# Kernel tuning notes

Measured on AMD Instinct MI355X. Metric: run time of the kernel, lower is better.

## Reference

```python
import jax, jax.numpy as jnp
import numpy as np

B, H, W, C = 8, 64, 64, 512
DQK = C // 8  # query/key channel dim from Conv2D(filters//8, 1)


def setup_inputs() -> dict:
    key = jax.random.key(0)
    ks = jax.random.split(key, 8)
    s_in = 1.0 / np.sqrt(C)
    x = jax.random.normal(ks[0], (B, H, W, C), dtype=jnp.float32)
    Wq = jax.random.normal(ks[1], (C, DQK), dtype=jnp.float32) * s_in
    bq = jnp.zeros((DQK,), dtype=jnp.float32)
    Wk = jax.random.normal(ks[2], (C, DQK), dtype=jnp.float32) * s_in
    bk = jnp.zeros((DQK,), dtype=jnp.float32)
    Wv = jax.random.normal(ks[3], (C, C), dtype=jnp.float32) * s_in
    bv = jnp.zeros((C,), dtype=jnp.float32)
    # gamma initialized to zeros in the original, but use a nonzero value so
    # the attention branch actually contributes to the output/gradients.
    gamma = jnp.ones((1,), dtype=jnp.float32) * 0.5
    return {"x": x, "Wq": Wq, "bq": bq, "Wk": Wk, "bk": bk,
            "Wv": Wv, "bv": bv, "gamma": gamma}


def reference(x, Wq, bq, Wk, bk, Wv, bv, gamma):
    b, h, w, c = x.shape
    n = h * w  # spatial_size
    xf = x.reshape(b, n, c)
    # 1x1 convs == per-pixel channel matmuls
    q = xf @ Wq + bq            # [B, N, C//8]
    k = xf @ Wk + bk            # [B, N, C//8]
    v = xf @ Wv + bv            # [B, N, C]
    # Dot(axes=-1): attn[b,i,j] = sum_d q[b,i,d] * k[b,j,d]
    attn = jnp.einsum('bid,bjd->bij', q, k)
    attn = jax.nn.softmax(attn, axis=-1)
    # Dot(axes=-2): out[b,j,c] = sum_i attn[b,i,j] * v[b,i,c]  (note transpose)
    out = jnp.einsum('bij,bic->bjc', attn, v)
    out = out.reshape(b, h, w, c)
    return gamma * out + x
```

## Files before the change

### kernel.cpp

```cpp
#include <hip/hip_runtime.h>
#include <hip/hip_bf16.h>
#include <cstdio>

typedef unsigned short u16;
typedef __attribute__((ext_vector_type(4))) float f32x4;
typedef __attribute__((ext_vector_type(8))) short s16x8;

#define LOG2E 1.4426950408889634f

__device__ __forceinline__ u16 bf16b(float f) {
  union { float f; unsigned u; } c; c.f = f;
  unsigned u = c.u;
  return (u16)((u + 0x7FFFu + ((u >> 16) & 1u)) >> 16);
}

__device__ __forceinline__ void load16(const void* g, void* l) {
  __builtin_amdgcn_global_load_lds(
      (const __attribute__((address_space(1))) void*)g,
      (__attribute__((address_space(3))) void*)l, 16, 0, 0);
}


__global__ __launch_bounds__(256) void cvt_all_k(const float* __restrict__ x,
                                                 const float* __restrict__ Wq,
                                                 const float* __restrict__ Wk,
                                                 const float* __restrict__ Wv,
                                                 u16* __restrict__ xb,
                                                 u16* __restrict__ Wcat) {
  int bid = blockIdx.x;
  if (bid < 16384) {
    long i = ((long)bid * 256 + threadIdx.x) * 4;
    float4 f = *(const float4*)&x[i];
    unsigned lo = (unsigned)bf16b(f.x) | ((unsigned)bf16b(f.y) << 16);
    unsigned hi = (unsigned)bf16b(f.z) | ((unsigned)bf16b(f.w) << 16);
    uint2 v; v.x = lo; v.y = hi;
    *(uint2*)&xb[i] = v;
  } else {
    int idx = (bid - 16384) * 256 + threadIdx.x;
    int nn = idx >> 9, k = idx & 511;
    float v;
    if (nn < 64)       v = Wq[k * 64 + nn];
    else if (nn < 128) v = Wk[k * 64 + (nn - 64)];
    else               v = Wv[k * 512 + (nn - 128)];
    Wcat[idx] = bf16b(v);
  }
}

__global__ __launch_bounds__(256, 2) void projGemm(
    const u16* __restrict__ A, const u16* __restrict__ B,
    u16* __restrict__ Qb, u16* __restrict__ Kb, u16* __restrict__ Vt,
    const float* __restrict__ bq, const float* __restrict__ bk,
    const float* __restrict__ bv) {
  constexpr int BM = 128, BN = 128, FM = 4, FN = 4;
  __shared__ __align__(16) u16 At[BM * 64];
  __shared__ __align__(16) u16 Bt[BN * 64];
  const int tid = threadIdx.x;
  const int lane = tid & 63, w = tid >> 6;
  const int wr = w >> 1, wc = w & 1;
  const int l15 = lane & 15, lhi = lane >> 4;
  const long m0 = (long)blockIdx.x * BM;
  const long n0 = (long)blockIdx.y * BN;

  f32x4 acc[FM][FN] = {};

  for (int k0 = 0; k0 < 512; k0 += 64) {
#pragma unroll
    for (int it = 0; it < 8; ++it) {
      int q = it * 256 + tid;
      if (q < BM * 8) {
        int row = q >> 3, c8 = q & 7;
        load16(A + (m0 + row) * 512 + k0 + c8 * 8, &At[q * 8]);
      } else {
        int q2 = q - BM * 8;
        int row = q2 >> 3, c8 = q2 & 7;
        load16(B + (n0 + row) * 512 + k0 + c8 * 8, &Bt[q2 * 8]);
      }
    }
    __syncthreads();
#pragma unroll
    for (int kk = 0; kk < 64; kk += 32) {
      s16x8 af[FM], bf[FN];
#pragma unroll
      for (int i = 0; i < FM; ++i)
        af[i] = *(const s16x8*)&At[(wr * 64 + i * 16 + l15) * 64 + kk + lhi * 8];
#pragma unroll
      for (int j = 0; j < FN; ++j)
        bf[j] = *(const s16x8*)&Bt[(wc * 64 + j * 16 + l15) * 64 + kk + lhi * 8];
#pragma unroll
      for (int i = 0; i < FM; ++i)
#pragma unroll
        for (int j = 0; j < FN; ++j)
          acc[i][j] = __builtin_amdgcn_mfma_f32_16x16x32_bf16(af[i], bf[j],
                                                              acc[i][j], 0, 0, 0);
    }
    __syncthreads();
  }

#pragma unroll
  for (int i = 0; i < FM; ++i) {
#pragma unroll
    for (int j = 0; j < FN; ++j) {
      long mm = m0 + wr * 64 + i * 16 + lhi * 4;
      long nn = n0 + wc * 64 + j * 16 + l15;
      if (nn < 64) {
        float bb = bq[nn];
#pragma unroll
        for (int r = 0; r < 4; ++r)
          Qb[(mm + r) * 64 + nn] = bf16b(acc[i][j][r] + bb);
      } else if (nn < 128) {
        float bb = bk[nn - 64];
#pragma unroll
        for (int r = 0; r < 4; ++r)
          Kb[(mm + r) * 64 + nn - 64] = bf16b(acc[i][j][r] + bb);
      } else {
        long c = nn - 128;
        float bb = bv[c];
        unsigned u01 = (unsigned)bf16b(acc[i][j][0] + bb) |
                       ((unsigned)bf16b(acc[i][j][1] + bb) << 16);
        unsigned u23 = (unsigned)bf16b(acc[i][j][2] + bb) |
                       ((unsigned)bf16b(acc[i][j][3] + bb) << 16);
        uint2 u; u.x = u01; u.y = u23;
        *(uint2*)&Vt[(mm >> 12) * 512 * 4096 + c * 4096 + (mm & 4095)] = u;
      }
    }
  }
}

__global__ __launch_bounds__(256, 2) void stats_k(const u16* __restrict__ Qb,
                                                  const u16* __restrict__ Kb,
                                                  float* __restrict__ m_part,
                                                  float* __restrict__ l_part) {
  const int b = blockIdx.z, jc = blockIdx.y;
  const long i0 = (long)blockIdx.x * 128;
  const u16* Q = Qb + (long)b * 4096 * 64;
  const u16* Kp = Kb + (long)b * 4096 * 64;
  __shared__ __align__(16) u16 Qt[128 * 64];
  __shared__ __align__(16) u16 Kt[128 * 64];
  const int tid = threadIdx.x, lane = tid & 63, w = tid >> 6;
  const int l15 = lane & 15, lhi = lane >> 4;

#pragma unroll
  for (int it = 0; it < 4; ++it) {
    int q = it * 256 + tid;
    int row = q >> 3, c8 = q & 7;
    load16(Q + (i0 + row) * 64 + c8 * 8, &Qt[q * 8]);
  }

  float mrun[2][4], lrun[2][4];
#pragma unroll
  for (int i = 0; i < 2; ++i)
#pragma unroll
    for (int r = 0; r < 4; ++r) { mrun[i][r] = -1e30f; lrun[i][r] = 0.f; }

  for (int jt = 0; jt < 8; ++jt) {
    long j0 = (long)jc * 1024 + jt * 128;
#pragma unroll
    for (int it = 0; it < 4; ++it) {
      int q = it * 256 + tid;
      int row = q >> 3, c8 = q & 7;
      load16(Kp + (j0 + row) * 64 + c8 * 8, &Kt[q * 8]);
    }
    __syncthreads();
    f32x4 acc[2][8] = {};
#pragma unroll
    for (int kk = 0; kk < 64; kk += 32) {
      s16x8 af[2], bf[8];
#pragma unroll
      for (int i = 0; i < 2; ++i)
        af[i] = *(const s16x8*)&Qt[(w * 32 + i * 16 + l15) * 64 + kk + lhi * 8];
#pragma unroll
      for (int j = 0; j < 8; ++j)
        bf[j] = *(const s16x8*)&Kt[(j * 16 + l15) * 64 + kk + lhi * 8];
#pragma unroll
      for (int i = 0; i < 2; ++i)
#pragma unroll
        for (int j = 0; j < 8; ++j)
          acc[i][j] = __builtin_amdgcn_mfma_f32_16x16x32_bf16(af[i], bf[j],
                                                              acc[i][j], 0, 0, 0);
    }
#pragma unroll
    for (int i = 0; i < 2; ++i)
#pragma unroll
      for (int r = 0; r < 4; ++r) {
        float tm = acc[i][0][r];
#pragma unroll
        for (int j = 1; j < 8; ++j) tm = fmaxf(tm, acc[i][j][r]);
        float mo = mrun[i][r];
        float mn = fmaxf(mo, tm);
        float s = 0.f;
#pragma unroll
        for (int j = 0; j < 8; ++j) s += __expf(acc[i][j][r] - mn);
        lrun[i][r] = lrun[i][r] * __expf(mo - mn) + s;
        mrun[i][r] = mn;
      }
    __syncthreads();
  }

#pragma unroll
  for (int i = 0; i < 2; ++i)
#pragma unroll
    for (int r = 0; r < 4; ++r) {
      float m = mrun[i][r], l = lrun[i][r];
#pragma unroll
      for (int d = 1; d < 16; d <<= 1) {
        float mo = __shfl_xor(m, d);
        float lo = __shfl_xor(l, d);
        float mn = fmaxf(m, mo);
        l = l * __expf(m - mn) + lo * __expf(mo - mn);
        m = mn;
      }
      if (l15 == 0) {
        long ig = i0 + w * 32 + i * 16 + lhi * 4 + r;
        long idx = ((long)(b * 4 + jc)) * 4096 + ig;
        m_part[idx] = m;
        l_part[idx] = l;
      }
    }
}

__global__ __launch_bounds__(256) void merge_k(const float* __restrict__ m_part,
                                               const float* __restrict__ l_part,
                                               float* __restrict__ mfin) {
  int idx = blockIdx.x * 256 + threadIdx.x;
  int b = idx >> 12, i = idx & 4095;
  float m = -1e30f, l = 0.f;
#pragma unroll
  for (int jc = 0; jc < 4; ++jc) {
    long o = ((long)(b * 4 + jc)) * 4096 + i;
    float mp = m_part[o], lp = l_part[o];
    float mn = fmaxf(m, mp);
    l = l * __expf(m - mn) + lp * __expf(mp - mn);
    m = mn;
  }
  mfin[idx] = fmaf(m, LOG2E, __log2f(l));
}

__global__ __launch_bounds__(512, 2) void fusedPV(
    const u16* __restrict__ Qb, const u16* __restrict__ Kb,
    const u16* __restrict__ Vt, const float* __restrict__ mfin,
    const float* __restrict__ x, const float* __restrict__ gamma,
    float* __restrict__ out) {
  __shared__ __align__(16) u16 Vc[2][512 * 64];
  __shared__ __align__(16) u16 Pl[2][128 * 64];
  const int tid = threadIdx.x, lane = tid & 63, w = tid >> 6;
  const int l15 = lane & 15, lhi = lane >> 4;
  const int wi = w & 1, wj = w >> 1;
  const int wjj = w & 1, wcc = w >> 1;
  const int s = blockIdx.x + 32 * blockIdx.z;
  const int pi = (s & 7) * 32 + (s >> 3);
  const int b = pi >> 5;
  const long j0 = (long)(pi & 31) * 128;
  const u16* Qg = Qb + (long)b * 4096 * 64;
  const u16* Kg = Kb + (long)b * 4096 * 64;
  const u16* Vg = Vt + (long)b * 512 * 4096;
  const float* mg = mfin + (long)b * 4096;
  const float gma = gamma[0];

#pragma unroll
  for (int p = 0; p < 2; ++p) {
    int q = p * 512 + tid;
    int r = q >> 3, col = q & 7, cg = col ^ (r & 7);
    load16(Kg + (j0 + r) * 64 + cg * 8,
           (char*)&Pl[0][0] + r * 128 + col * 16);
  }
  asm volatile("s_waitcnt vmcnt(0) lgkmcnt(0)\n\ts_barrier" ::: "memory");
  s16x8 kf[2][2];
#pragma unroll
  for (int fj = 0; fj < 2; ++fj)
#pragma unroll
    for (int kx = 0; kx < 2; ++kx) {
      int r = wj * 32 + fj * 16 + l15;
      kf[fj][kx] = *(const s16x8*)((const char*)&Pl[0][0] + r * 128 +
                                   (((kx * 32 + lhi * 8) * 2) ^ ((r & 7) << 4)));
    }
  __syncthreads();

  f32x4 acc2[4][8] = {};
  s16x8 qf[2][2];
  f32x4 mv[2];

#pragma unroll
  for (int fi = 0; fi < 2; ++fi) {
#pragma unroll
    for (int kx = 0; kx < 2; ++kx)
      qf[fi][kx] = *(const s16x8*)&Qg[(long)(wi * 32 + fi * 16 + l15) * 64 +
                                      kx * 32 + lhi * 8];
    mv[fi] = *(const f32x4*)&mg[wi * 32 + fi * 16 + lhi * 4];
  }
#pragma unroll
  for (int p = 0; p < 8; ++p) {
    int q = p * 512 + tid;
    int r = q >> 3, col = q & 7, cg = col ^ (r & 7);
    load16(Vg + (long)r * 4096 + cg * 8,
           (char*)&Vc[0][0] + r * 128 + col * 16);
  }
#pragma unroll
  for (int fi = 0; fi < 2; ++fi) {
    f32x4 a1[2] = {};
#pragma unroll
    for (int kx = 0; kx < 2; ++kx)
#pragma unroll
      for (int fj = 0; fj < 2; ++fj)
        a1[fj] = __builtin_amdgcn_mfma_f32_16x16x32_bf16(qf[fi][kx],
                                                         kf[fj][kx], a1[fj],
                                                         0, 0, 0);
    const int i0l = wi * 32 + fi * 16 + lhi * 4;
#pragma unroll
    for (int fj = 0; fj < 2; ++fj) {
      int j = wj * 32 + fj * 16 + l15;
      float p0 = __builtin_amdgcn_exp2f(fmaf(a1[fj][0], LOG2E, -mv[fi][0]));
      float p1 = __builtin_amdgcn_exp2f(fmaf(a1[fj][1], LOG2E, -mv[fi][1]));
      float p2 = __builtin_amdgcn_exp2f(fmaf(a1[fj][2], LOG2E, -mv[fi][2]));
      float p3 = __builtin_amdgcn_exp2f(fmaf(a1[fj][3], LOG2E, -mv[fi][3]));
      uint2 u;
      u.x = (unsigned)bf16b(p0) | ((unsigned)bf16b(p1) << 16);
      u.y = (unsigned)bf16b(p2) | ((unsigned)bf16b(p3) << 16);
      *(uint2*)((char*)&Pl[0][0] + j * 128 + ((i0l * 2) ^ ((j & 7) << 4))) = u;
    }
  }

  for (int t = 0; t < 64; ++t) {
    const char* plc = (const char*)&Pl[t & 1][0];
    char* pln = (char*)&Pl[(t + 1) & 1][0];
    const char* vcc = (const char*)&Vc[t & 1][0];
    asm volatile("s_waitcnt vmcnt(0) lgkmcnt(0)\n\ts_barrier" ::: "memory");
    if (t < 63) {
      const long i2 = (long)(t + 1) * 64;
#pragma unroll
      for (int fi = 0; fi < 2; ++fi) {
#pragma unroll
        for (int kx = 0; kx < 2; ++kx)
          qf[fi][kx] = *(const s16x8*)&Qg[(i2 + wi * 32 + fi * 16 + l15) * 64 +
                                          kx * 32 + lhi * 8];
        mv[fi] = *(const f32x4*)&mg[i2 + wi * 32 + fi * 16 + lhi * 4];
      }
#pragma unroll
      for (int p = 0; p < 8; ++p) {
        int q = p * 512 + tid;
        int r = q >> 3, col = q & 7, cg = col ^ (r & 7);
        load16(Vg + (long)r * 4096 + i2 + cg * 8,
               (char*)&Vc[(t + 1) & 1][0] + r * 128 + col * 16);
      }
    }
    __builtin_amdgcn_sched_barrier(0);
    __builtin_amdgcn_s_setprio(1);
#pragma unroll
    for (int kx = 0; kx < 2; ++kx) {
      s16x8 pa[4];
#pragma unroll
      for (int fm = 0; fm < 4; ++fm) {
        int r = wjj * 64 + fm * 16 + l15;
        pa[fm] = *(const s16x8*)(plc + r * 128 +
                                 (((kx * 32 + lhi * 8) * 2) ^ ((r & 7) << 4)));
      }
#pragma unroll
      for (int fn = 0; fn < 8; ++fn) {
        int r = wcc * 128 + fn * 16 + l15;
        s16x8 vb = *(const s16x8*)(vcc + r * 128 +
                                   (((kx * 32 + lhi * 8) * 2) ^ ((r & 7) << 4)));
#pragma unroll
        for (int fm = 0; fm < 4; ++fm)
          acc2[fm][fn] = __builtin_amdgcn_mfma_f32_16x16x32_bf16(
              pa[fm], vb, acc2[fm][fn], 0, 0, 0);
      }
    }
    __builtin_amdgcn_s_setprio(0);
    if (t < 63) {
#pragma unroll
      for (int fi = 0; fi < 2; ++fi) {
        f32x4 a1[2] = {};
#pragma unroll
        for (int kx = 0; kx < 2; ++kx)
#pragma unroll
          for (int fj = 0; fj < 2; ++fj)
            a1[fj] = __builtin_amdgcn_mfma_f32_16x16x32_bf16(qf[fi][kx],
                                                             kf[fj][kx],
                                                             a1[fj], 0, 0, 0);
        const int i0l = wi * 32 + fi * 16 + lhi * 4;
#pragma unroll
        for (int fj = 0; fj < 2; ++fj) {
          int j = wj * 32 + fj * 16 + l15;
          float p0 = __builtin_amdgcn_exp2f(fmaf(a1[fj][0], LOG2E, -mv[fi][0]));
          float p1 = __builtin_amdgcn_exp2f(fmaf(a1[fj][1], LOG2E, -mv[fi][1]));
          float p2 = __builtin_amdgcn_exp2f(fmaf(a1[fj][2], LOG2E, -mv[fi][2]));
          float p3 = __builtin_amdgcn_exp2f(fmaf(a1[fj][3], LOG2E, -mv[fi][3]));
          uint2 u;
          u.x = (unsigned)bf16b(p0) | ((unsigned)bf16b(p1) << 16);
          u.y = (unsigned)bf16b(p2) | ((unsigned)bf16b(p3) << 16);
          *(uint2*)(pln + j * 128 + ((i0l * 2) ^ ((j & 7) << 4))) = u;
        }
      }
    }
  }

#pragma unroll
  for (int fm = 0; fm < 4; ++fm) {
#pragma unroll
    for (int fn = 0; fn < 8; ++fn) {
      long j = j0 + wjj * 64 + fm * 16 + lhi * 4;
      long c = wcc * 128 + fn * 16 + l15;
#pragma unroll
      for (int r = 0; r < 4; ++r) {
        long o = ((long)b * 4096 + j + r) * 512 + c;
        out[o] = gma * acc2[fm][fn][r] + x[o];
      }
    }
  }
}


extern "C" void kernel_launch(void* const* d_in, const int* in_sizes, int n_in,
                              void* d_out, int out_size, void* d_ws,
                              size_t ws_size, hipStream_t stream) {
  const float* x = (const float*)d_in[0];
  const float* Wq = (const float*)d_in[1];
  const float* bq = (const float*)d_in[2];
  const float* Wk = (const float*)d_in[3];
  const float* bk = (const float*)d_in[4];
  const float* Wv = (const float*)d_in[5];
  const float* bv = (const float*)d_in[6];
  const float* gamma = (const float*)d_in[7];
  float* out = (float*)d_out;

  char* ws = (char*)d_ws;
  size_t off = 0;
  auto alloc = [&](size_t bytes) {
    char* p = ws + off;
    off += (bytes + 255) & ~(size_t)255;
    return p;
  };
  u16* xb = (u16*)alloc((size_t)32768 * 512 * 2);
  u16* Wcat = (u16*)alloc((size_t)640 * 512 * 2);
  u16* Qb = (u16*)alloc((size_t)8 * 4096 * 64 * 2);
  u16* Kb = (u16*)alloc((size_t)8 * 4096 * 64 * 2);
  u16* Vt = (u16*)alloc((size_t)8 * 512 * 4096 * 2);
  float* m_part = (float*)alloc((size_t)8 * 4 * 4096 * 4);
  float* l_part = (float*)alloc((size_t)8 * 4 * 4096 * 4);
  float* mfin = (float*)alloc((size_t)8 * 4096 * 4);
  if (off > ws_size) {
    fprintf(stderr, "kernel_launch: ws too small: need %zu have %zu\n", off,
            ws_size);
    return;
  }

  cvt_all_k<<<16384 + 1280, 256, 0, stream>>>(x, Wq, Wk, Wv, xb, Wcat);
  projGemm<<<dim3(256, 5, 1), 256, 0, stream>>>(xb, Wcat, Qb, Kb, Vt, bq, bk,
                                                bv);
  stats_k<<<dim3(32, 4, 8), 256, 0, stream>>>(Qb, Kb, m_part, l_part);
  merge_k<<<128, 256, 0, stream>>>(m_part, l_part, mfin);
  fusedPV<<<dim3(32, 1, 8), 512, 0, stream>>>(Qb, Kb, Vt, mfin, x, gamma,
                                              out);
}
```

Measured before the change: 290.8 us.

## Interleave P-tile softmax compute with PV MFMA phases using split barriers

Splits the P·V MFMA block into four phases (two k-halves × two column halves) and interleaves the next tile's QK^T MFMA, exp2 and P stores between them, separated by raw s_barrier instructions. The aim is to overlap softmax ALU/exp work and LDS traffic with matrix-core work across waves, ping-pong style. It adds extra workgroup barriers per iteration, which cost synchronisation time and could reduce overlap if the waves end up in lockstep.

```diff
diff --git a/kernel.cpp b/kernel.cpp
--- a/kernel.cpp
+++ b/kernel.cpp
@@ -343,52 +343,123 @@
       }
     }
     __builtin_amdgcn_sched_barrier(0);
+
+    s16x8 pa[4], vb[4];
+#pragma unroll
+    for (int fm = 0; fm < 4; ++fm) {
+      int r = wjj * 64 + fm * 16 + l15;
+      pa[fm] = *(const s16x8*)(plc + r * 128 +
+                               (((0 + lhi * 8) * 2) ^ ((r & 7) << 4)));
+    }
+#pragma unroll
+    for (int fn = 0; fn < 4; ++fn) {
+      int r = wcc * 128 + fn * 16 + l15;
+      vb[fn] = *(const s16x8*)(vcc + r * 128 +
+                               (((0 + lhi * 8) * 2) ^ ((r & 7) << 4)));
+    }
     __builtin_amdgcn_s_setprio(1);
 #pragma unroll
-    for (int kx = 0; kx < 2; ++kx) {
-      s16x8 pa[4];
-#pragma unroll
-      for (int fm = 0; fm < 4; ++fm) {
-        int r = wjj * 64 + fm * 16 + l15;
-        pa[fm] = *(const s16x8*)(plc + r * 128 +
-                                 (((kx * 32 + lhi * 8) * 2) ^ ((r & 7) << 4)));
-      }
-#pragma unroll
-      for (int fn = 0; fn < 8; ++fn) {
-        int r = wcc * 128 + fn * 16 + l15;
-        s16x8 vb = *(const s16x8*)(vcc + r * 128 +
-                                   (((kx * 32 + lhi * 8) * 2) ^ ((r & 7) << 4)));
-#pragma unroll
-        for (int fm = 0; fm < 4; ++fm)
-          acc2[fm][fn] = __builtin_amdgcn_mfma_f32_16x16x32_bf16(
-              pa[fm], vb, acc2[fm][fn], 0, 0, 0);
-      }
-    }
+    for (int fn = 0; fn < 4; ++fn)
+#pragma unroll
+      for (int fm = 0; fm < 4; ++fm)
+        acc2[fm][fn] = __builtin_amdgcn_mfma_f32_16x16x32_bf16(
+            pa[fm], vb[fn], acc2[fm][fn], 0, 0, 0);
+    __builtin_amdgcn_s_setprio(0);
+    asm volatile("s_barrier" ::: "memory");
+#pragma unroll
+    for (int fn = 0; fn < 4; ++fn) {
+      int r = wcc * 128 + (4 + fn) * 16 + l15;
+      vb[fn] = *(const s16x8*)(vcc + r * 128 +
+                               (((0 + lhi * 8) * 2) ^ ((r & 7) << 4)));
+    }
+    __builtin_amdgcn_s_setprio(1);
+#pragma unroll
+    for (int fn = 0; fn < 4; ++fn)
+#pragma unroll
+      for (int fm = 0; fm < 4; ++fm)
+        acc2[fm][4 + fn] = __builtin_amdgcn_mfma_f32_16x16x32_bf16(
+            pa[fm], vb[fn], acc2[fm][4 + fn], 0, 0, 0);
+    __builtin_amdgcn_s_setprio(0);
+    asm volatile("s_barrier" ::: "memory");
+    if (t < 63) {
+      f32x4 a1[2] = {};
+#pragma unroll
+      for (int kx = 0; kx < 2; ++kx)
+#pragma unroll
+        for (int fj = 0; fj < 2; ++fj)
+          a1[fj] = __builtin_amdgcn_mfma_f32_16x16x32_bf16(qf[0][kx],
+                                                           kf[fj][kx], a1[fj],
+                                                           0, 0, 0);
+      const int i0l = wi * 32 + lhi * 4;
+#pragma unroll
+      for (int fj = 0; fj < 2; ++fj) {
+        int j = wj * 32 + fj * 16 + l15;
+        float p0 = __builtin_amdgcn_exp2f(fmaf(a1[fj][0], LOG2E, -mv[0][0]));
+        float p1 = __builtin_amdgcn_exp2f(fmaf(a1[fj][1], LOG2E, -mv[0][1]));
+        float p2 = __builtin_amdgcn_exp2f(fmaf(a1[fj][2], LOG2E, -mv[0][2]));
+        float p3 = __builtin_amdgcn_exp2f(fmaf(a1[fj][3], LOG2E, -mv[0][3]));
+        uint2 u;
+        u.x = (unsigned)bf16b(p0) | ((unsigned)bf16b(p1) << 16);
+        u.y = (unsigned)bf16b(p2) | ((unsigned)bf16b(p3) << 16);
+        *(uint2*)(pln + j * 128 + ((i0l * 2) ^ ((j & 7) << 4))) = u;
+      }
+    }
+#pragma unroll
+    for (int fm = 0; fm < 4; ++fm) {
+      int r = wjj * 64 + fm * 16 + l15;
+      pa[fm] = *(const s16x8*)(plc + r * 128 +
+                               (((32 + lhi * 8) * 2) ^ ((r & 7) << 4)));
+    }
+#pragma unroll
+    for (int fn = 0; fn < 4; ++fn) {
+      int r = wcc * 128 + fn * 16 + l15;
+      vb[fn] = *(const s16x8*)(vcc + r * 128 +
+                               (((32 + lhi * 8) * 2) ^ ((r & 7) << 4)));
+    }
+    __builtin_amdgcn_s_setprio(1);
+#pragma unroll
+    for (int fn = 0; fn < 4; ++fn)
+#pragma unroll
+      for (int fm = 0; fm < 4; ++fm)
+        acc2[fm][fn] = __builtin_amdgcn_mfma_f32_16x16x32_bf16(
+            pa[fm], vb[fn], acc2[fm][fn], 0, 0, 0);
+    __builtin_amdgcn_s_setprio(0);
+    asm volatile("s_barrier" ::: "memory");
+#pragma unroll
+    for (int fn = 0; fn < 4; ++fn) {
+      int r = wcc * 128 + (4 + fn) * 16 + l15;
+      vb[fn] = *(const s16x8*)(vcc + r * 128 +
+                               (((32 + lhi * 8) * 2) ^ ((r & 7) << 4)));
+    }
+    __builtin_amdgcn_s_setprio(1);
+#pragma unroll
+    for (int fn = 0; fn < 4; ++fn)
+#pragma unroll
+      for (int fm = 0; fm < 4; ++fm)
+        acc2[fm][4 + fn] = __builtin_amdgcn_mfma_f32_16x16x32_bf16(
+            pa[fm], vb[fn], acc2[fm][4 + fn], 0, 0, 0);
     __builtin_amdgcn_s_setprio(0);
     if (t < 63) {
-#pragma unroll
-      for (int fi = 0; fi < 2; ++fi) {
-        f32x4 a1[2] = {};
-#pragma unroll
-        for (int kx = 0; kx < 2; ++kx)
-#pragma unroll
-          for (int fj = 0; fj < 2; ++fj)
-            a1[fj] = __builtin_amdgcn_mfma_f32_16x16x32_bf16(qf[fi][kx],
-                                                             kf[fj][kx],
-                                                             a1[fj], 0, 0, 0);
-        const int i0l = wi * 32 + fi * 16 + lhi * 4;
-#pragma unroll
-        for (int fj = 0; fj < 2; ++fj) {
-          int j = wj * 32 + fj * 16 + l15;
-          float p0 = __builtin_amdgcn_exp2f(fmaf(a1[fj][0], LOG2E, -mv[fi][0]));
-          float p1 = __builtin_amdgcn_exp2f(fmaf(a1[fj][1], LOG2E, -mv[fi][1]));
-          float p2 = __builtin_amdgcn_exp2f(fmaf(a1[fj][2], LOG2E, -mv[fi][2]));
-          float p3 = __builtin_amdgcn_exp2f(fmaf(a1[fj][3], LOG2E, -mv[fi][3]));
-          uint2 u;
-          u.x = (unsigned)bf16b(p0) | ((unsigned)bf16b(p1) << 16);
-          u.y = (unsigned)bf16b(p2) | ((unsigned)bf16b(p3) << 16);
-          *(uint2*)(pln + j * 128 + ((i0l * 2) ^ ((j & 7) << 4))) = u;
-        }
+      f32x4 a1[2] = {};
+#pragma unroll
+      for (int kx = 0; kx < 2; ++kx)
+#pragma unroll
+        for (int fj = 0; fj < 2; ++fj)
+          a1[fj] = __builtin_amdgcn_mfma_f32_16x16x32_bf16(qf[1][kx],
+                                                           kf[fj][kx], a1[fj],
+                                                           0, 0, 0);
+      const int i0l = wi * 32 + 16 + lhi * 4;
+#pragma unroll
+      for (int fj = 0; fj < 2; ++fj) {
+        int j = wj * 32 + fj * 16 + l15;
+        float p0 = __builtin_amdgcn_exp2f(fmaf(a1[fj][0], LOG2E, -mv[1][0]));
+        float p1 = __builtin_amdgcn_exp2f(fmaf(a1[fj][1], LOG2E, -mv[1][1]));
+        float p2 = __builtin_amdgcn_exp2f(fmaf(a1[fj][2], LOG2E, -mv[1][2]));
+        float p3 = __builtin_amdgcn_exp2f(fmaf(a1[fj][3], LOG2E, -mv[1][3]));
+        uint2 u;
+        u.x = (unsigned)bf16b(p0) | ((unsigned)bf16b(p1) << 16);
+        u.y = (unsigned)bf16b(p2) | ((unsigned)bf16b(p3) << 16);
+        *(uint2*)(pln + j * 128 + ((i0l * 2) ^ ((j & 7) << 4))) = u;
       }
     }
   }
```

After: 321.6 us. 1.11x slower.
